# Kernel optimization log

Hardware: AMD Instinct MI355X
Metric: run time of the kernel (lower is better)

Reference implementation:

```python
import jax, jax.numpy as jnp
import numpy as np

N = 50000          # total points
C = 256            # channels
H = 8              # heads
D = C // H         # head dim = 32
W = 256            # window size
STRIDE = 128
LENGTHS = [12500, 12500, 12500, 12500]
HID = 512          # ffn hidden = 2.0 * C
EPS = 1e-5


def _build_windows():
    """numpy port of build_windows_1d: returns (M, W) indices and bool mask."""
    idxs, masks = [], []
    start = 0
    for L in LENGTHS:
        n_windows = (L - 1) // STRIDE + 1
        for i in range(n_windows):
            s = i * STRIDE
            b = min(L, s + W)
            cur_len = b - s
            loc = np.arange(s, b, dtype=np.int32) + start
            if W - cur_len > 0:
                loc = np.concatenate([loc, np.full(W - cur_len, loc[-1], dtype=np.int32)])
            m = np.zeros(W, dtype=bool)
            m[:cur_len] = True
            idxs.append(loc)
            masks.append(m)
        start += L
    return np.stack(idxs, 0), np.stack(masks, 0)


def setup_inputs() -> dict:
    key = jax.random.key(0)
    ks = jax.random.split(key, 8)
    def p(k, shape):
        return jax.random.normal(k, shape, dtype=jnp.float32) * 0.02
    win_idx_np, win_mask_np = _build_windows()
    return {
        "x": jax.random.normal(ks[0], (N, C), dtype=jnp.float32),
        "win_idx": jnp.asarray(win_idx_np, dtype=jnp.int32),
        "win_mask": jnp.asarray(win_mask_np),
        "norm1_g": jnp.ones((C,), jnp.float32), "norm1_b": jnp.zeros((C,), jnp.float32),
        "qkv_w": p(ks[1], (C, 3 * C)),
        "proj_w": p(ks[2], (C, C)), "proj_b": jnp.zeros((C,), jnp.float32),
        "ca_norm_g": jnp.ones((C,), jnp.float32), "ca_norm_b": jnp.zeros((C,), jnp.float32),
        "ca_qkv_w": p(ks[3], (C, 3 * C)), "ca_qkv_b": jnp.zeros((3 * C,), jnp.float32),
        "ca_proj_w": p(ks[4], (C, C)), "ca_proj_b": jnp.zeros((C,), jnp.float32),
        "norm2_g": jnp.ones((C,), jnp.float32), "norm2_b": jnp.zeros((C,), jnp.float32),
        "ffn_w1": p(ks[5], (C, HID)), "ffn_b1": jnp.zeros((HID,), jnp.float32),
        "ffn_ln_g": jnp.ones((HID,), jnp.float32), "ffn_ln_b": jnp.zeros((HID,), jnp.float32),
        "ffn_w2": p(ks[6], (HID, C)), "ffn_b2": jnp.zeros((C,), jnp.float32),
    }


def _ln(x, g, b):
    m = jnp.mean(x, axis=-1, keepdims=True)
    v = jnp.mean((x - m) ** 2, axis=-1, keepdims=True)
    return (x - m) * jax.lax.rsqrt(v + EPS) * g + b


def reference(x, win_idx, win_mask,
              norm1_g, norm1_b, qkv_w, proj_w, proj_b,
              ca_norm_g, ca_norm_b, ca_qkv_w, ca_qkv_b, ca_proj_w, ca_proj_b,
              norm2_g, norm2_b, ffn_w1, ffn_b1, ffn_ln_g, ffn_ln_b, ffn_w2, ffn_b2):
    M, Wn = win_idx.shape
    scale = D ** -0.5
    maskf = win_mask[..., None].astype(x.dtype)          # [M, W, 1]

    x_in = _ln(x, norm1_g, norm1_b)                      # [N, C]
    xw = x_in[win_idx]                                   # gather windows [M, W, C]

    # --- Stream A: per-window SDPA ---
    qkv = xw @ qkv_w                                     # [M, W, 3C]
    q, k, v = [t.reshape(M, Wn, H, D).transpose(0, 2, 1, 3)
               for t in jnp.split(qkv, 3, axis=-1)]      # each [M, H, W, D]
    scores = jnp.einsum('mhqd,mhkd->mhqk', q, k) * scale
    scores = jnp.where(win_mask[:, None, None, :], scores, -jnp.inf)
    attn = jax.nn.softmax(scores, axis=-1)
    out = jnp.einsum('mhqk,mhkd->mhqd', attn, v).transpose(0, 2, 1, 3).reshape(M, Wn, C)
    out = (out @ proj_w + proj_b) * maskf                # masked per-window output

    # --- Stream B: centroid attention over M window centroids ---
    wc = jnp.maximum(win_mask.sum(-1, keepdims=True).astype(x.dtype), 1.0)  # [M, 1]
    cent = (xw * maskf).sum(1) / wc                      # [M, C]
    cx = _ln(cent, ca_norm_g, ca_norm_b)
    cqkv = cx @ ca_qkv_w + ca_qkv_b
    cq, ck, cv = [t.reshape(M, H, D).transpose(1, 0, 2)
                  for t in jnp.split(cqkv, 3, axis=-1)]  # each [H, M, D]
    cs = jnp.einsum('hqd,hkd->hqk', cq, ck) * scale
    co = jnp.einsum('hqk,hkd->hqd', jax.nn.softmax(cs, -1), cv)
    co = co.transpose(1, 0, 2).reshape(M, C)
    cent_out = cent + co @ ca_proj_w + ca_proj_b         # residual + proj

    gctx = cent_out[:, None, :] * maskf                  # broadcast global ctx [M, W, C]

    # --- scatter-add back with overlap averaging ---
    total = (out + gctx).reshape(-1, C)
    flat_idx = win_idx.reshape(-1)
    y = jnp.zeros_like(x).at[flat_idx].add(total)
    counts = jnp.zeros((x.shape[0], 1), x.dtype).at[flat_idx].add(
        win_mask.reshape(-1, 1).astype(x.dtype))
    x_out = x + y / jnp.maximum(counts, 1.0)

    # --- FFN (LayerNorm variant) ---
    h1 = _ln(x_out, norm2_g, norm2_b) @ ffn_w1 + ffn_b1
    h1 = jax.nn.relu(_ln(h1, ffn_ln_g, ffn_ln_b))
    return x_out + h1 @ ffn_w2 + ffn_b2
```

## Files before the change

### kernel.cpp

```cpp
#include <hip/hip_runtime.h>

typedef unsigned short ushort;
typedef unsigned int uint;
typedef __attribute__((ext_vector_type(4))) float f32x4;
typedef __attribute__((ext_vector_type(16))) float f32x16;
typedef __attribute__((ext_vector_type(8))) short bf16x8;
typedef __attribute__((ext_vector_type(4))) uint uint32x4;
typedef __attribute__((ext_vector_type(2))) uint uint2v;

#define NPTS 50000
#define C 256
#define CH3 768
#define H 8
#define D 32
#define WW 256
#define HID 512
#define EPSV 1e-5f
#define QK_SCALE 0.17677669529663687f
#define LOG2E 1.4426950408889634f
#define SC_LOG2 (QK_SCALE * LOG2E)

#define BM 128
#define BN 128
#define BK 64
#define NGEMM_QKV 2346
#define NCENT 392
#define NATT 3136
#define NPROJ 1568

#if __has_builtin(__builtin_amdgcn_exp2f)
#define EXP2R(x) __builtin_amdgcn_exp2f(x)
#else
#define EXP2R(x) exp2f(x)
#endif

__device__ inline float bf2f(ushort u) { uint i = ((uint)u) << 16; float f; __builtin_memcpy(&f, &i, 4); return f; }
__device__ inline float bflo(uint u) { uint i = u << 16; float f; __builtin_memcpy(&f, &i, 4); return f; }
__device__ inline float bfhi(uint u) { uint i = u & 0xffff0000u; float f; __builtin_memcpy(&f, &i, 4); return f; }
__device__ inline ushort f2bf(float f) {
  uint i; __builtin_memcpy(&i, &f, 4);
  uint r = i + 0x7fffu + ((i >> 16) & 1u);
  return (ushort)(r >> 16);
}
__device__ inline uint pk2bf(float a, float b) { return (uint)f2bf(a) | ((uint)f2bf(b) << 16); }

__device__ __forceinline__ void gload16(const ushort* g, const ushort* l) {
  __builtin_amdgcn_global_load_lds(
      (const __attribute__((address_space(1))) unsigned int*)(unsigned long long)g,
      (__attribute__((address_space(3))) unsigned int*)(unsigned int)(unsigned long long)l,
      16, 0, 0);
}

__device__ __forceinline__ int xcd_swz(int orig, int nwg) {
  int q8 = nwg >> 3, r8 = nwg & 7;
  int xcd = orig & 7, sub = orig >> 3;
  return (xcd < r8 ? xcd * (q8 + 1) : r8 * (q8 + 1) + (xcd - r8) * q8) + sub;
}

#define BLOCK_REDUCE_2(sv, s2v)                                            \
  {                                                                        \
    _Pragma("unroll")                                                      \
    for (int o_ = 1; o_ < 64; o_ <<= 1) {                                  \
      sv  += __shfl_xor(sv, o_);                                           \
      s2v += __shfl_xor(s2v, o_);                                          \
    }                                                                      \
    __shared__ float ls_[4], ls2_[4];                                      \
    int wid_ = threadIdx.x >> 6;                                           \
    if ((threadIdx.x & 63) == 0) { ls_[wid_] = sv; ls2_[wid_] = s2v; }     \
    __syncthreads();                                                       \
    sv  = ls_[0] + ls_[1] + ls_[2] + ls_[3];                               \
    s2v = ls2_[0] + ls2_[1] + ls2_[2] + ls2_[3];                           \
  }

template <int EPI>
__device__ __forceinline__ void gemm_body(ushort* SMEM, int bid,
                                          const ushort* __restrict__ A,
                                          const ushort* __restrict__ Bt,
                                          void* __restrict__ outp,
                                          const float* __restrict__ bias,
                                          int Mrows, int Ncols, int K) {
  ushort* As = SMEM;
  ushort* Bs = SMEM + BM * BK;
  int t = threadIdx.x;
  int nbn = Ncols >> 7;
  int bm = bid / nbn, bn = bid - bm * nbn;
  int l = t & 63, wv = t >> 6;
  int wr = wv >> 1, wcid = wv & 1;
  int l15 = l & 15, l4 = l >> 4;
  int lr = l >> 3;
  int csrc = ((l & 7) ^ lr) << 3;
  f32x4 acc[4][4];
#pragma unroll
  for (int i = 0; i < 4; ++i)
#pragma unroll
    for (int j = 0; j < 4; ++j) acc[i][j] = (f32x4){0.f, 0.f, 0.f, 0.f};

  int nks = K >> 6;
  for (int ks = 0; ks < nks; ++ks) {
    if (ks) __syncthreads();
#pragma unroll
    for (int i = 0; i < 4; ++i) {
      int rloc = wv * 8 + lr + i * 32;
      int growA = min(bm * BM + rloc, Mrows - 1);
      gload16(&A[(size_t)growA * K + (ks << 6) + csrc], &As[(wv * 8 + i * 32) * BK]);
      gload16(&Bt[(size_t)(bn * BN + rloc) * K + (ks << 6) + csrc], &Bs[(wv * 8 + i * 32) * BK]);
    }
    __syncthreads();
#pragma unroll
    for (int kk = 0; kk < 2; ++kk) {
      bf16x8 af[4], bfr[4];
#pragma unroll
      for (int i = 0; i < 4; ++i) {
        int ra = wr * 64 + i * 16 + l15;
        int ca = (l4 + kk * 4) ^ (ra & 7);
        af[i] = *(const bf16x8*)&As[ra * BK + (ca << 3)];
        int rb = wcid * 64 + i * 16 + l15;
        int cb = (l4 + kk * 4) ^ (rb & 7);
        bfr[i] = *(const bf16x8*)&Bs[rb * BK + (cb << 3)];
      }
      __builtin_amdgcn_s_setprio(1);
#pragma unroll
      for (int i = 0; i < 4; ++i)
#pragma unroll
        for (int j = 0; j < 4; ++j)
          acc[i][j] = __builtin_amdgcn_mfma_f32_16x16x32_bf16(af[i], bfr[j], acc[i][j], 0, 0, 0);
      __builtin_amdgcn_s_setprio(0);
    }
  }

  const int CS = 136;
  ushort* Cs = SMEM;
#pragma unroll
  for (int pass = 0; pass < 2; ++pass) {
    __syncthreads();
    if (wr == pass) {
#pragma unroll
      for (int i = 0; i < 4; ++i)
#pragma unroll
        for (int j = 0; j < 4; ++j)
#pragma unroll
          for (int r = 0; r < 4; ++r) {
            int rl = i * 16 + l4 * 4 + r;
            int cl = wcid * 64 + j * 16 + l15;
            float v = acc[i][j][r];
            if (EPI >= 1) v += bias[bn * BN + cl];
            Cs[rl * CS + cl] = f2bf(v);
          }
    }
    __syncthreads();
    int rl = t >> 2;
    int cq = (t & 3) * 32;
    int grow = bm * BM + pass * 64 + rl;
    if (grow < Mrows) {
      if (EPI <= 1) {
        ushort* orow = (ushort*)outp + (size_t)grow * Ncols + bn * BN + cq;
#pragma unroll
        for (int s = 0; s < 4; ++s)
          *(uint4*)(orow + s * 8) = *(const uint4*)&Cs[rl * CS + cq + s * 8];
      } else {
        float* orow = (float*)outp + (size_t)grow * Ncols + bn * BN + cq;
#pragma unroll
        for (int s = 0; s < 8; ++s) {
          float4 ov = *(float4*)(orow + s * 4);
          const ushort* cp = &Cs[rl * CS + cq + s * 4];
          ov.x += bf2f(cp[0]); ov.y += bf2f(cp[1]);
          ov.z += bf2f(cp[2]); ov.w += bf2f(cp[3]);
          *(float4*)(orow + s * 4) = ov;
        }
      }
    }
  }
}

template <int EPI>
__global__ __launch_bounds__(256, 4) void gemm_bf16(
    const ushort* __restrict__ A, const ushort* __restrict__ Bt, void* __restrict__ outp,
    const float* __restrict__ bias, int Mrows, int Ncols, int K) {
  __shared__ ushort SMEM[(BM + BN) * BK];
  int bid = xcd_swz(blockIdx.x, gridDim.x);
  gemm_body<EPI>(SMEM, bid, A, Bt, outp, bias, Mrows, Ncols, K);
}

__global__ __launch_bounds__(256) void pre_kernel(
    const float* __restrict__ qkv_w, const float* __restrict__ proj_w,
    const float* __restrict__ w1, const float* __restrict__ w2,
    ushort* __restrict__ qkv_wt, ushort* __restrict__ proj_wt,
    ushort* __restrict__ w1t, ushort* __restrict__ w2t,
    const float* __restrict__ x, const float* __restrict__ g, const float* __restrict__ b,
    ushort* __restrict__ xout) {
  int bid = blockIdx.x;
  if (bid < 128) {
    __shared__ float tile[64][65];
    const float* w; ushort* wt; int K, N, boff; float scale; int n_hi;
    if (bid < 48)      { w = qkv_w;  wt = qkv_wt;  K = C;   N = CH3; boff = 0;  scale = SC_LOG2; n_hi = C; }
    else if (bid < 64) { w = proj_w; wt = proj_wt; K = C;   N = C;   boff = 48; scale = 1.f; n_hi = 0; }
    else if (bid < 96) { w = w1;     wt = w1t;     K = C;   N = HID; boff = 64; scale = 1.f; n_hi = 0; }
    else               { w = w2;     wt = w2t;     K = HID; N = C;   boff = 96; scale = 1.f; n_hi = 0; }
    int lb = bid - boff;
    int nbn = N >> 6;
    int bk = lb / nbn, bn = lb - bk * nbn;
    int c = threadIdx.x & 63, r4 = threadIdx.x >> 6;
#pragma unroll
    for (int rr = 0; rr < 16; ++rr) {
      int r = rr * 4 + r4;
      tile[r][c] = w[(size_t)(bk * 64 + r) * N + bn * 64 + c];
    }
    __syncthreads();
#pragma unroll
    for (int rr = 0; rr < 16; ++rr) {
      int r = rr * 4 + r4;
      int n = bn * 64 + r;
      float s = (n < n_hi) ? scale : 1.f;
      wt[(size_t)n * K + bk * 64 + c] = f2bf(tile[c][r] * s);
    }
  } else {
    int wv = threadIdx.x >> 6, lane = threadIdx.x & 63;
    int row = (bid - 128) * 4 + wv;
    float4 v = ((const float4*)(x + (size_t)row * C))[lane];
    float s = v.x + v.y + v.z + v.w;
    float s2 = v.x * v.x + v.y * v.y + v.z * v.z + v.w * v.w;
#pragma unroll
    for (int o = 1; o < 64; o <<= 1) { s += __shfl_xor(s, o); s2 += __shfl_xor(s2, o); }
    float mean = s * (1.0f / C);
    float var = s2 * (1.0f / C) - mean * mean;
    float rs = rsqrtf(var + EPSV);
    float4 gv = ((const float4*)g)[lane];
    float4 bv = ((const float4*)b)[lane];
    uint2 pk;
    pk.x = pk2bf((v.x - mean) * rs * gv.x + bv.x, (v.y - mean) * rs * gv.y + bv.y);
    pk.y = pk2bf((v.z - mean) * rs * gv.z + bv.z, (v.w - mean) * rs * gv.w + bv.w);
    ((uint2*)(xout + (size_t)row * C))[lane] = pk;
  }
}

__global__ __launch_bounds__(256, 4) void qkv_cent_kernel(
    const ushort* __restrict__ xb, const int* __restrict__ win_idx,
    const float* __restrict__ lng, const float* __restrict__ lnb,
    const float* __restrict__ caw, const float* __restrict__ cab,
    float* __restrict__ cent, float* __restrict__ cqkv, float* __restrict__ kT,
    int* __restrict__ wc_i, const ushort* __restrict__ qkv_wt, ushort* __restrict__ qkvb, int M) {
  __shared__ ushort SMEM[(BM + BN) * BK];
  int bid = blockIdx.x;
  if (bid < NCENT) {
    float* fbase = (float*)SMEM;
    float (*red)[257] = (float(*)[257])fbase;
    float* cxl = fbase + 8 * 257;
    int m = bid, t = threadIdx.x;
    int i0 = win_idx[m * WW];
    int iL = win_idx[m * WW + WW - 1];
    int wc = iL - i0 + 1;
    if (t == 0) wc_i[m] = wc;
    int rg = t >> 5, cg = t & 31;
    float acc[8] = {0.f, 0.f, 0.f, 0.f, 0.f, 0.f, 0.f, 0.f};
    for (int r = rg; r < wc; r += 8) {
      uint4 u = *(const uint4*)(xb + (size_t)(i0 + r) * C + cg * 8);
      acc[0] += bflo(u.x); acc[1] += bfhi(u.x);
      acc[2] += bflo(u.y); acc[3] += bfhi(u.y);
      acc[4] += bflo(u.z); acc[5] += bfhi(u.z);
      acc[6] += bflo(u.w); acc[7] += bfhi(u.w);
    }
#pragma unroll
    for (int j = 0; j < 8; ++j) red[rg][cg * 8 + j] = acc[j];
    __syncthreads();
    float sum = red[0][t];
#pragma unroll
    for (int k = 1; k < 8; ++k) sum += red[k][t];
    float cv = sum / (float)wc;
    cent[m * C + t] = cv;
    float s = cv, s2 = cv * cv;
    BLOCK_REDUCE_2(s, s2);
    float mean = s * (1.0f / C);
    float var = s2 * (1.0f / C) - mean * mean;
    float rs = rsqrtf(var + EPSV);
    cxl[t] = (cv - mean) * rs * lng[t] + lnb[t];
    __syncthreads();
    for (int j = t; j < CH3; j += 256) {
      float a = cab[j];
      for (int c2 = 0; c2 < C; ++c2) a += cxl[c2] * caw[(size_t)c2 * CH3 + j];
      cqkv[(size_t)m * CH3 + j] = a;
      if (j >= C && j < 2 * C) kT[(size_t)(j - C) * M + m] = a;
    }
  } else {
    int g = xcd_swz(bid - NCENT, NGEMM_QKV);
    gemm_body<0>(SMEM, g, xb, qkv_wt, qkvb, nullptr, NPTS, CH3, C);
  }
}

__global__ __launch_bounds__(256) void attn_cent_kernel(
    const ushort* __restrict__ qkv, const int* __restrict__ win_idx,
    const int* __restrict__ wc_i, ushort* __restrict__ ao,
    const float* __restrict__ cqkv, const float* __restrict__ kT,
    float* __restrict__ co, int* __restrict__ slots, int M) {
  __shared__ char SM[37376];
  int bid = blockIdx.x;
  int t = threadIdx.x;

  if (bid < NCENT) {
    float (*p_lds)[400] = (float(*)[400])(float*)SM;
    int wv = t >> 6, lane = t & 63;
    int mq = bid;
#pragma unroll
    for (int pp = 0; pp < 2; ++pp) {
      int h = wv * 2 + pp;
      const float* qp = cqkv + (size_t)mq * CH3 + h * D;
      float q[D];
#pragma unroll
      for (int d = 0; d < D; ++d) q[d] = qp[d] * SC_LOG2;
      float s[7];
      float mi = -3.0e38f;
#pragma unroll
      for (int j = 0; j < 7; ++j) {
        int mk = lane + 64 * j;
        s[j] = -3.0e38f;
        if (mk < M) {
          float a = 0.f;
#pragma unroll
          for (int d = 0; d < D; ++d) a += q[d] * kT[(size_t)(h * D + d) * M + mk];
          s[j] = a;
          mi = fmaxf(mi, a);
        }
      }
#pragma unroll
      for (int off = 1; off < 64; off <<= 1) mi = fmaxf(mi, __shfl_xor(mi, off));
      float li = 0.f;
#pragma unroll
      for (int j = 0; j < 7; ++j) {
        int mk = lane + 64 * j;
        if (mk < M) { float pv = EXP2R(s[j] - mi); li += pv; p_lds[h][mk] = pv; }
      }
#pragma unroll
      for (int off = 1; off < 64; off <<= 1) li += __shfl_xor(li, off);
      int d = lane & 31, hpp = lane >> 5;
      int half = (M + 1) / 2;
      int k0 = hpp * half, k1 = min(M, k0 + half);
      float o = 0.f;
      for (int k = k0; k < k1; ++k)
        o += p_lds[h][k] * cqkv[(size_t)k * CH3 + 2 * C + h * D + d];
      o += __shfl_xor(o, 32);
      if (lane < 32) co[(size_t)mq * C + h * D + d] = o / li;
    }
    return;
  }
  if (bid < 2 * NCENT) {
    int m = bid - NCENT;
    int wc = wc_i[m];
    int i0 = win_idx[m * WW];
    if (t < wc) slots[2 * (i0 + t) + (t >= 128 ? 0 : 1)] = m * WW + t;
    return;
  }

  ushort* K_lds = (ushort*)SM;
  uint* Vt = (uint*)(SM + 20480);
  int abid = xcd_swz(bid - 2 * NCENT, NATT);
  int m = abid >> 3, h = abid & 7;
  int wcv = wc_i[m];
  int i0 = win_idx[m * WW];
  int lane = t & 63, wq = t >> 6;
  int l31 = lane & 31, hp = lane >> 5;

  bf16x8 qf[2][2];
#pragma unroll
  for (int qb = 0; qb < 2; ++qb) {
    int qrow = i0 + min(wq * 64 + qb * 32 + l31, wcv - 1);
#pragma unroll
    for (int c = 0; c < 2; ++c)
      qf[qb][c] = *(const bf16x8*)(qkv + (size_t)qrow * CH3 + h * D + c * 16 + hp * 8);
  }

  if (t >= 128) {
    int base = (t - 128) * 2;
#pragma unroll
    for (int rr = 0; rr < 2; ++rr) {
      int row = base + rr;
      const uint4* src = (const uint4*)(qkv + (size_t)(i0 + min(row, wcv - 1)) * CH3 + C + h * D);
      *(uint4*)&K_lds[row * 40 + 0]  = src[0];
      *(uint4*)&K_lds[row * 40 + 8]  = src[1];
      *(uint4*)&K_lds[row * 40 + 16] = src[2];
      *(uint4*)&K_lds[row * 40 + 24] = src[3];
    }
  } else {
    int k0 = t * 2;
    const uint* s0 = (const uint*)(qkv + (size_t)(i0 + min(k0, wcv - 1)) * CH3 + 2 * C + h * D);
    const uint* s1 = (const uint*)(qkv + (size_t)(i0 + min(k0 + 1, wcv - 1)) * CH3 + 2 * C + h * D);
#pragma unroll
    for (int w2 = 0; w2 < 16; ++w2) {
      uint a = s0[w2], b = s1[w2];
      Vt[(2 * w2) * 132 + t] = (a & 0xffffu) | (b << 16);
      Vt[(2 * w2 + 1) * 132 + t] = (a >> 16) | (b & 0xffff0000u);
    }
  }
  __syncthreads();

  const f32x16 zv = {0.f, 0.f, 0.f, 0.f, 0.f, 0.f, 0.f, 0.f,
                     0.f, 0.f, 0.f, 0.f, 0.f, 0.f, 0.f, 0.f};
  f32x16 O0 = zv, O1 = zv;
  float l0 = 0.f, l1 = 0.f;
  int ntile = (wcv + 31) >> 5;

  for (int kt = 0; kt < ntile; ++kt) {
    int kbase = kt * 32;
    bf16x8 ka0 = *(const bf16x8*)&K_lds[(kbase + l31) * 40 + hp * 8];
    bf16x8 ka1 = *(const bf16x8*)&K_lds[(kbase + l31) * 40 + 16 + hp * 8];
    uint4 v0raw = *(const uint4*)&Vt[l31 * 132 + kt * 16 + hp * 4];
    uint4 v1raw = *(const uint4*)&Vt[l31 * 132 + kt * 16 + 8 + hp * 4];
    bf16x8 vb0 = __builtin_bit_cast(bf16x8, v0raw);
    bf16x8 vb1 = __builtin_bit_cast(bf16x8, v1raw);
    bool partial = (kbase + 32 > wcv);

    auto qbody = [&](const bf16x8& q0, const bf16x8& q1, f32x16& O, float& lq) {
      __builtin_amdgcn_s_setprio(1);
      f32x16 st = __builtin_amdgcn_mfma_f32_32x32x16_bf16(ka0, q0, zv, 0, 0, 0);
      st = __builtin_amdgcn_mfma_f32_32x32x16_bf16(ka1, q1, st, 0, 0, 0);
      __builtin_amdgcn_s_setprio(0);
      if (partial) {
        int kb_h = kbase + 4 * hp;
#pragma unroll
        for (int r = 0; r < 16; ++r) {
          int crow = (r & 3) + 8 * (r >> 2);
          st[r] = (kb_h + crow >= wcv) ? -3.0e38f : st[r];
        }
      }
      float p[16];
      float ls = 0.f;
#pragma unroll
      for (int r = 0; r < 16; ++r) { p[r] = EXP2R(st[r]); ls += p[r]; }
      lq += ls;
      uint w[8];
#pragma unroll
      for (int i = 0; i < 8; ++i) {
        uint o;
        asm("v_cvt_pk_bf16_f32 %0, %1, %2" : "=v"(o) : "v"(p[2 * i]), "v"(p[2 * i + 1]));
        w[i] = o;
      }
#if __has_builtin(__builtin_amdgcn_permlane32_swap)
      uint2v s02 = __builtin_amdgcn_permlane32_swap(w[0], w[2], false, false);
      uint2v s13 = __builtin_amdgcn_permlane32_swap(w[1], w[3], false, false);
      uint2v s46 = __builtin_amdgcn_permlane32_swap(w[4], w[6], false, false);
      uint2v s57 = __builtin_amdgcn_permlane32_swap(w[5], w[7], false, false);
      uint32x4 pa0u = {s02.x, s13.x, s02.y, s13.y};
      uint32x4 pa1u = {s46.x, s57.x, s46.y, s57.y};
#else
      uint sw0 = __shfl_xor((int)w[0], 32), sw1 = __shfl_xor((int)w[1], 32);
      uint sw2 = __shfl_xor((int)w[2], 32), sw3 = __shfl_xor((int)w[3], 32);
      uint sw4 = __shfl_xor((int)w[4], 32), sw5 = __shfl_xor((int)w[5], 32);
      uint sw6 = __shfl_xor((int)w[6], 32), sw7 = __shfl_xor((int)w[7], 32);
      uint32x4 pa0u = {hp ? sw2 : w[0], hp ? sw3 : w[1], hp ? w[2] : sw0, hp ? w[3] : sw1};
      uint32x4 pa1u = {hp ? sw6 : w[4], hp ? sw7 : w[5], hp ? w[6] : sw4, hp ? w[7] : sw5};
#endif
      bf16x8 pa0 = __builtin_bit_cast(bf16x8, pa0u);
      bf16x8 pa1 = __builtin_bit_cast(bf16x8, pa1u);
      __builtin_amdgcn_s_setprio(1);
      O = __builtin_amdgcn_mfma_f32_32x32x16_bf16(pa0, vb0, O, 0, 0, 0);
      O = __builtin_amdgcn_mfma_f32_32x32x16_bf16(pa1, vb1, O, 0, 0, 0);
      __builtin_amdgcn_s_setprio(0);
    };
    qbody(qf[0][0], qf[0][1], O0, l0);
    qbody(qf[1][0], qf[1][1], O1, l1);
  }

  auto epi = [&](f32x16& O, float lq, int qb) {
    float lt = lq + __shfl_xor(lq, 32);
    float inv = 1.f / lt;
#pragma unroll
    for (int r = 0; r < 16; ++r) {
      int qi = (r & 3) + 8 * (r >> 2) + 4 * hp;
      float iv = __shfl(inv, qi);
      int row = m * WW + wq * 64 + qb * 32 + qi;
      ao[(size_t)row * C + h * D + l31] = f2bf(O[r] * iv);
    }
  };
  epi(O0, l0, 0);
  epi(O1, l1, 1);
}

__global__ __launch_bounds__(256, 4) void proj_cent_kernel(
    const ushort* __restrict__ aob, const ushort* __restrict__ proj_wt,
    ushort* __restrict__ pout, const float* __restrict__ proj_b,
    const float* __restrict__ co, const float* __restrict__ cent,
    const float* __restrict__ pw, const float* __restrict__ pb,
    float* __restrict__ cent_o, int M) {
  __shared__ ushort SMEM[(BM + BN) * BK];
  int bid = blockIdx.x;
  if (bid < NCENT) {
    float* co_lds = (float*)SMEM;
    int mq = bid, t = threadIdx.x;
    co_lds[t] = co[(size_t)mq * C + t];
    __syncthreads();
    float a = pb[t] + cent[(size_t)mq * C + t];
    for (int k = 0; k < C; ++k) a += co_lds[k] * pw[(size_t)k * C + t];
    cent_o[(size_t)mq * C + t] = a;
    return;
  }
  int g = xcd_swz(bid - NCENT, NPROJ);
  gemm_body<1>(SMEM, g, aob, proj_wt, pout, proj_b, M * WW, C, C);
}

__global__ __launch_bounds__(256) void combine_ln_kernel(
    const float* __restrict__ x, const int* __restrict__ slots,
    const ushort* __restrict__ pout, const float* __restrict__ cent_o,
    const float* __restrict__ g, const float* __restrict__ b,
    float* __restrict__ xout, ushort* __restrict__ lnx) {
  int wv = threadIdx.x >> 6, lane = threadIdx.x & 63;
  int i = blockIdx.x * 4 + wv;
  int e0 = slots[2 * i], e1 = slots[2 * i + 1];
  float4 xv = ((const float4*)(x + (size_t)i * C))[lane];
  float a0 = 0.f, a1 = 0.f, a2 = 0.f, a3 = 0.f, cnt = 0.f;
  if (e0 >= 0) {
    uint2 pv = ((const uint2*)(pout + (size_t)e0 * C))[lane];
    float4 cv = ((const float4*)(cent_o + (size_t)(e0 >> 8) * C))[lane];
    a0 += bflo(pv.x) + cv.x; a1 += bfhi(pv.x) + cv.y;
    a2 += bflo(pv.y) + cv.z; a3 += bfhi(pv.y) + cv.w;
    cnt += 1.f;
  }
  if (e1 >= 0) {
    uint2 pv = ((const uint2*)(pout + (size_t)e1 * C))[lane];
    float4 cv = ((const float4*)(cent_o + (size_t)(e1 >> 8) * C))[lane];
    a0 += bflo(pv.x) + cv.x; a1 += bfhi(pv.x) + cv.y;
    a2 += bflo(pv.y) + cv.z; a3 += bfhi(pv.y) + cv.w;
    cnt += 1.f;
  }
  float inv = cnt > 0.f ? 1.f / cnt : 0.f;
  float o0 = xv.x + a0 * inv, o1 = xv.y + a1 * inv;
  float o2 = xv.z + a2 * inv, o3 = xv.w + a3 * inv;
  float s = o0 + o1 + o2 + o3;
  float s2 = o0 * o0 + o1 * o1 + o2 * o2 + o3 * o3;
#pragma unroll
  for (int o = 1; o < 64; o <<= 1) { s += __shfl_xor(s, o); s2 += __shfl_xor(s2, o); }
  float mean = s * (1.0f / C);
  float var = s2 * (1.0f / C) - mean * mean;
  float rs = rsqrtf(var + EPSV);
  ((float4*)(xout + (size_t)i * C))[lane] = make_float4(o0, o1, o2, o3);
  float4 gv = ((const float4*)g)[lane];
  float4 bv = ((const float4*)b)[lane];
  uint2 pk;
  pk.x = pk2bf((o0 - mean) * rs * gv.x + bv.x, (o1 - mean) * rs * gv.y + bv.y);
  pk.y = pk2bf((o2 - mean) * rs * gv.z + bv.z, (o3 - mean) * rs * gv.w + bv.w);
  ((uint2*)(lnx + (size_t)i * C))[lane] = pk;
}

__global__ __launch_bounds__(256) void hln_relu_kernel(ushort* __restrict__ h,
                                                       const float* __restrict__ g,
                                                       const float* __restrict__ b) {
  int wv = threadIdx.x >> 6, lane = threadIdx.x & 63;
  int i = blockIdx.x * 4 + wv;
  uint4 u = ((const uint4*)(h + (size_t)i * HID))[lane];
  float v[8] = {bflo(u.x), bfhi(u.x), bflo(u.y), bfhi(u.y),
                bflo(u.z), bfhi(u.z), bflo(u.w), bfhi(u.w)};
  float s = 0.f, s2 = 0.f;
#pragma unroll
  for (int j = 0; j < 8; ++j) { s += v[j]; s2 += v[j] * v[j]; }
#pragma unroll
  for (int o = 1; o < 64; o <<= 1) { s += __shfl_xor(s, o); s2 += __shfl_xor(s2, o); }
  float mean = s * (1.0f / HID);
  float var = s2 * (1.0f / HID) - mean * mean;
  float rs = rsqrtf(var + EPSV);
  float4 g0 = ((const float4*)g)[lane * 2], g1 = ((const float4*)g)[lane * 2 + 1];
  float4 b0 = ((const float4*)b)[lane * 2], b1 = ((const float4*)b)[lane * 2 + 1];
  float ga[8] = {g0.x, g0.y, g0.z, g0.w, g1.x, g1.y, g1.z, g1.w};
  float ba[8] = {b0.x, b0.y, b0.z, b0.w, b1.x, b1.y, b1.z, b1.w};
  float r[8];
#pragma unroll
  for (int j = 0; j < 8; ++j) r[j] = fmaxf((v[j] - mean) * rs * ga[j] + ba[j], 0.f);
  uint4 outu = make_uint4(pk2bf(r[0], r[1]), pk2bf(r[2], r[3]),
                          pk2bf(r[4], r[5]), pk2bf(r[6], r[7]));
  ((uint4*)(h + (size_t)i * HID))[lane] = outu;
}

extern "C" void kernel_launch(void* const* d_in, const int* in_sizes, int n_in,
                              void* d_out, int out_size, void* d_ws, size_t ws_size,
                              hipStream_t stream) {
  (void)n_in; (void)ws_size; (void)out_size;
  const float* x         = (const float*)d_in[0];
  const int*   win_idx   = (const int*)d_in[1];
  const float* norm1_g   = (const float*)d_in[3];
  const float* norm1_b   = (const float*)d_in[4];
  const float* qkv_w     = (const float*)d_in[5];
  const float* proj_w    = (const float*)d_in[6];
  const float* proj_b    = (const float*)d_in[7];
  const float* ca_norm_g = (const float*)d_in[8];
  const float* ca_norm_b = (const float*)d_in[9];
  const float* ca_qkv_w  = (const float*)d_in[10];
  const float* ca_qkv_b  = (const float*)d_in[11];
  const float* ca_proj_w = (const float*)d_in[12];
  const float* ca_proj_b = (const float*)d_in[13];
  const float* norm2_g   = (const float*)d_in[14];
  const float* norm2_b   = (const float*)d_in[15];
  const float* ffn_w1    = (const float*)d_in[16];
  const float* ffn_b1    = (const float*)d_in[17];
  const float* ffn_ln_g  = (const float*)d_in[18];
  const float* ffn_ln_b  = (const float*)d_in[19];
  const float* ffn_w2    = (const float*)d_in[20];
  const float* ffn_b2    = (const float*)d_in[21];

  const int M = in_sizes[1] / WW;

  char* p = (char*)d_ws;
  auto alloc = [&](size_t bytes) { char* r = p; p += (bytes + 255) & ~(size_t)255; return r; };
  ushort* x_in_b = (ushort*)alloc((size_t)NPTS * C * 2);
  ushort* qkvb   = (ushort*)alloc((size_t)NPTS * CH3 * 2);
  ushort* aob    = (ushort*)alloc((size_t)M * WW * C * 2);
  ushort* pout   = (ushort*)alloc((size_t)M * WW * C * 2);
  int*   slots   = (int*)  alloc((size_t)NPTS * 2 * 4);
  int*   wc_i    = (int*)  alloc((size_t)M * 4);
  float* cent    = (float*)alloc((size_t)M * C * 4);
  float* cqkv    = (float*)alloc((size_t)M * CH3 * 4);
  float* kT      = (float*)alloc((size_t)C * M * 4);
  float* co      = (float*)alloc((size_t)M * C * 4);
  float* cent_o  = (float*)alloc((size_t)M * C * 4);
  ushort* qkv_wt = (ushort*)alloc((size_t)CH3 * C * 2);
  ushort* proj_wt= (ushort*)alloc((size_t)C * C * 2);
  ushort* w1t    = (ushort*)alloc((size_t)HID * C * 2);
  ushort* w2t    = (ushort*)alloc((size_t)C * HID * 2);
  float* yout    = (float*)d_out;

  hipMemsetAsync(slots, 0xFF, (size_t)NPTS * 2 * 4, stream);

  pre_kernel<<<128 + NPTS / 4, 256, 0, stream>>>(
      qkv_w, proj_w, ffn_w1, ffn_w2, qkv_wt, proj_wt, w1t, w2t,
      x, norm1_g, norm1_b, x_in_b);

  qkv_cent_kernel<<<NCENT + NGEMM_QKV, 256, 0, stream>>>(
      x_in_b, win_idx, ca_norm_g, ca_norm_b, ca_qkv_w, ca_qkv_b,
      cent, cqkv, kT, wc_i, qkv_wt, qkvb, M);

  attn_cent_kernel<<<2 * NCENT + NATT, 256, 0, stream>>>(
      qkvb, win_idx, wc_i, aob, cqkv, kT, co, slots, M);

  proj_cent_kernel<<<NCENT + NPROJ, 256, 0, stream>>>(
      aob, proj_wt, pout, proj_b, co, cent, ca_proj_w, ca_proj_b, cent_o, M);

  ushort* lnx = x_in_b;
  combine_ln_kernel<<<NPTS / 4, 256, 0, stream>>>(x, slots, pout, cent_o, norm2_g, norm2_b,
                                                  yout, lnx);
  ushort* h1 = qkvb;
  const int gm = (NPTS + BM - 1) / BM;
  gemm_bf16<1><<<gm * (HID / BN), 256, 0, stream>>>(lnx, w1t, h1, ffn_b1,
                                                    NPTS, HID, C);
  hln_relu_kernel<<<NPTS / 4, 256, 0, stream>>>(h1, ffn_ln_g, ffn_ln_b);
  gemm_bf16<2><<<gm * (C / BN), 256, 0, stream>>>(h1, w2t, yout, ffn_b2,
                                                  NPTS, C, HID);
}
```

Before: 387.8 us.

## Use 512-thread blocks in window attention, one 32-query tile per wave

Doubles the attention kernel's block size to 512 threads so each of 8 waves handles one 32-row query tile (instead of 4 waves with two tiles each). The centroid branch now gives each wave a single head rather than looping over two. K and V staging is split across more threads. This raises parallelism and cuts per-wave serial work and register pressure, at the cost of more threads per block and fewer independent MFMA chains per wave for latency hiding. The slot-writing branch now has idle threads.

```diff
diff --git a/kernel.cpp b/kernel.cpp
--- a/kernel.cpp
+++ b/kernel.cpp
@@ -286,7 +286,7 @@
   }
 }
 
-__global__ __launch_bounds__(256) void attn_cent_kernel(
+__global__ __launch_bounds__(512) void attn_cent_kernel(
     const ushort* __restrict__ qkv, const int* __restrict__ win_idx,
     const int* __restrict__ wc_i, ushort* __restrict__ ao,
     const float* __restrict__ cqkv, const float* __restrict__ kT,
@@ -294,51 +294,49 @@
   __shared__ char SM[37376];
   int bid = blockIdx.x;
   int t = threadIdx.x;
+  int wavei = t >> 6, lane = t & 63;
+  int l31 = lane & 31, hp = lane >> 5;
 
   if (bid < NCENT) {
     float (*p_lds)[400] = (float(*)[400])(float*)SM;
-    int wv = t >> 6, lane = t & 63;
     int mq = bid;
-#pragma unroll
-    for (int pp = 0; pp < 2; ++pp) {
-      int h = wv * 2 + pp;
-      const float* qp = cqkv + (size_t)mq * CH3 + h * D;
-      float q[D];
-#pragma unroll
-      for (int d = 0; d < D; ++d) q[d] = qp[d] * SC_LOG2;
-      float s[7];
-      float mi = -3.0e38f;
-#pragma unroll
-      for (int j = 0; j < 7; ++j) {
-        int mk = lane + 64 * j;
-        s[j] = -3.0e38f;
-        if (mk < M) {
-          float a = 0.f;
-#pragma unroll
-          for (int d = 0; d < D; ++d) a += q[d] * kT[(size_t)(h * D + d) * M + mk];
-          s[j] = a;
-          mi = fmaxf(mi, a);
-        }
+    int h = wavei;
+    const float* qp = cqkv + (size_t)mq * CH3 + h * D;
+    float q[D];
+#pragma unroll
+    for (int d = 0; d < D; ++d) q[d] = qp[d] * SC_LOG2;
+    float s[7];
+    float mi = -3.0e38f;
+#pragma unroll
+    for (int j = 0; j < 7; ++j) {
+      int mk = lane + 64 * j;
+      s[j] = -3.0e38f;
+      if (mk < M) {
+        float a = 0.f;
+#pragma unroll
+        for (int d = 0; d < D; ++d) a += q[d] * kT[(size_t)(h * D + d) * M + mk];
+        s[j] = a;
+        mi = fmaxf(mi, a);
       }
-#pragma unroll
-      for (int off = 1; off < 64; off <<= 1) mi = fmaxf(mi, __shfl_xor(mi, off));
-      float li = 0.f;
-#pragma unroll
-      for (int j = 0; j < 7; ++j) {
-        int mk = lane + 64 * j;
-        if (mk < M) { float pv = EXP2R(s[j] - mi); li += pv; p_lds[h][mk] = pv; }
-      }
-#pragma unroll
-      for (int off = 1; off < 64; off <<= 1) li += __shfl_xor(li, off);
-      int d = lane & 31, hpp = lane >> 5;
-      int half = (M + 1) / 2;
-      int k0 = hpp * half, k1 = min(M, k0 + half);
-      float o = 0.f;
-      for (int k = k0; k < k1; ++k)
-        o += p_lds[h][k] * cqkv[(size_t)k * CH3 + 2 * C + h * D + d];
-      o += __shfl_xor(o, 32);
-      if (lane < 32) co[(size_t)mq * C + h * D + d] = o / li;
-    }
+    }
+#pragma unroll
+    for (int off = 1; off < 64; off <<= 1) mi = fmaxf(mi, __shfl_xor(mi, off));
+    float li = 0.f;
+#pragma unroll
+    for (int j = 0; j < 7; ++j) {
+      int mk = lane + 64 * j;
+      if (mk < M) { float pv = EXP2R(s[j] - mi); li += pv; p_lds[h][mk] = pv; }
+    }
+#pragma unroll
+    for (int off = 1; off < 64; off <<= 1) li += __shfl_xor(li, off);
+    int d = lane & 31, hpp = lane >> 5;
+    int half = (M + 1) / 2;
+    int k0 = hpp * half, k1 = min(M, k0 + half);
+    float o = 0.f;
+    for (int k = k0; k < k1; ++k)
+      o += p_lds[h][k] * cqkv[(size_t)k * CH3 + 2 * C + h * D + d];
+    o += __shfl_xor(o, 32);
+    if (lane < 32) co[(size_t)mq * C + h * D + d] = o / li;
     return;
   }
   if (bid < 2 * NCENT) {
@@ -355,30 +353,22 @@
   int m = abid >> 3, h = abid & 7;
   int wcv = wc_i[m];
   int i0 = win_idx[m * WW];
-  int lane = t & 63, wq = t >> 6;
-  int l31 = lane & 31, hp = lane >> 5;
-
-  bf16x8 qf[2][2];
-#pragma unroll
-  for (int qb = 0; qb < 2; ++qb) {
-    int qrow = i0 + min(wq * 64 + qb * 32 + l31, wcv - 1);
-#pragma unroll
-    for (int c = 0; c < 2; ++c)
-      qf[qb][c] = *(const bf16x8*)(qkv + (size_t)qrow * CH3 + h * D + c * 16 + hp * 8);
-  }
-
-  if (t >= 128) {
-    int base = (t - 128) * 2;
-#pragma unroll
-    for (int rr = 0; rr < 2; ++rr) {
-      int row = base + rr;
-      const uint4* src = (const uint4*)(qkv + (size_t)(i0 + min(row, wcv - 1)) * CH3 + C + h * D);
-      *(uint4*)&K_lds[row * 40 + 0]  = src[0];
-      *(uint4*)&K_lds[row * 40 + 8]  = src[1];
-      *(uint4*)&K_lds[row * 40 + 16] = src[2];
-      *(uint4*)&K_lds[row * 40 + 24] = src[3];
-    }
-  } else {
+
+  bf16x8 qf0, qf1;
+  {
+    int qrow = i0 + min(wavei * 32 + l31, wcv - 1);
+    qf0 = *(const bf16x8*)(qkv + (size_t)qrow * CH3 + h * D + hp * 8);
+    qf1 = *(const bf16x8*)(qkv + (size_t)qrow * CH3 + h * D + 16 + hp * 8);
+  }
+
+  if (t >= 256) {
+    int row = t - 256;
+    const uint4* src = (const uint4*)(qkv + (size_t)(i0 + min(row, wcv - 1)) * CH3 + C + h * D);
+    *(uint4*)&K_lds[row * 40 + 0]  = src[0];
+    *(uint4*)&K_lds[row * 40 + 8]  = src[1];
+    *(uint4*)&K_lds[row * 40 + 16] = src[2];
+    *(uint4*)&K_lds[row * 40 + 24] = src[3];
+  } else if (t < 128) {
     int k0 = t * 2;
     const uint* s0 = (const uint*)(qkv + (size_t)(i0 + min(k0, wcv - 1)) * CH3 + 2 * C + h * D);
     const uint* s1 = (const uint*)(qkv + (size_t)(i0 + min(k0 + 1, wcv - 1)) * CH3 + 2 * C + h * D);
@@ -393,84 +383,76 @@
 
   const f32x16 zv = {0.f, 0.f, 0.f, 0.f, 0.f, 0.f, 0.f, 0.f,
                      0.f, 0.f, 0.f, 0.f, 0.f, 0.f, 0.f, 0.f};
-  f32x16 O0 = zv, O1 = zv;
-  float l0 = 0.f, l1 = 0.f;
+  f32x16 O = zv;
+  float lq = 0.f;
   int ntile = (wcv + 31) >> 5;
 
   for (int kt = 0; kt < ntile; ++kt) {
     int kbase = kt * 32;
-    bf16x8 ka0 = *(const bf16x8*)&K_lds[(kbase + l31) * 40 + hp * 8];
-    bf16x8 ka1 = *(const bf16x8*)&K_lds[(kbase + l31) * 40 + 16 + hp * 8];
+    int rowk = kbase + l31;
+    bf16x8 ka0 = *(const bf16x8*)&K_lds[rowk * 40 + hp * 8];
+    bf16x8 ka1 = *(const bf16x8*)&K_lds[rowk * 40 + 16 + hp * 8];
     uint4 v0raw = *(const uint4*)&Vt[l31 * 132 + kt * 16 + hp * 4];
     uint4 v1raw = *(const uint4*)&Vt[l31 * 132 + kt * 16 + 8 + hp * 4];
     bf16x8 vb0 = __builtin_bit_cast(bf16x8, v0raw);
     bf16x8 vb1 = __builtin_bit_cast(bf16x8, v1raw);
     bool partial = (kbase + 32 > wcv);
 
-    auto qbody = [&](const bf16x8& q0, const bf16x8& q1, f32x16& O, float& lq) {
-      __builtin_amdgcn_s_setprio(1);
-      f32x16 st = __builtin_amdgcn_mfma_f32_32x32x16_bf16(ka0, q0, zv, 0, 0, 0);
-      st = __builtin_amdgcn_mfma_f32_32x32x16_bf16(ka1, q1, st, 0, 0, 0);
-      __builtin_amdgcn_s_setprio(0);
-      if (partial) {
-        int kb_h = kbase + 4 * hp;
-#pragma unroll
-        for (int r = 0; r < 16; ++r) {
-          int crow = (r & 3) + 8 * (r >> 2);
-          st[r] = (kb_h + crow >= wcv) ? -3.0e38f : st[r];
-        }
+    __builtin_amdgcn_s_setprio(1);
+    f32x16 st = __builtin_amdgcn_mfma_f32_32x32x16_bf16(ka0, qf0, zv, 0, 0, 0);
+    st = __builtin_amdgcn_mfma_f32_32x32x16_bf16(ka1, qf1, st, 0, 0, 0);
+    __builtin_amdgcn_s_setprio(0);
+    if (partial) {
+      int kb_h = kbase + 4 * hp;
+#pragma unroll
+      for (int r = 0; r < 16; ++r) {
+        int crow = (r & 3) + 8 * (r >> 2);
+        st[r] = (kb_h + crow >= wcv) ? -3.0e38f : st[r];
       }
-      float p[16];
-      float ls = 0.f;
-#pragma unroll
-      for (int r = 0; r < 16; ++r) { p[r] = EXP2R(st[r]); ls += p[r]; }
-      lq += ls;
-      uint w[8];
-#pragma unroll
-      for (int i = 0; i < 8; ++i) {
-        uint o;
-        asm("v_cvt_pk_bf16_f32 %0, %1, %2" : "=v"(o) : "v"(p[2 * i]), "v"(p[2 * i + 1]));
-        w[i] = o;
-      }
+    }
+    float ls = 0.f;
+#pragma unroll
+    for (int r = 0; r < 16; ++r) { st[r] = EXP2R(st[r]); ls += st[r]; }
+    lq += ls;
+    uint w[8];
+#pragma unroll
+    for (int i = 0; i < 8; ++i) {
+      uint o;
+      asm("v_cvt_pk_bf16_f32 %0, %1, %2" : "=v"(o) : "v"(st[2 * i]), "v"(st[2 * i + 1]));
+      w[i] = o;
+    }
 #if __has_builtin(__builtin_amdgcn_permlane32_swap)
-      uint2v s02 = __builtin_amdgcn_permlane32_swap(w[0], w[2], false, false);
-      uint2v s13 = __builtin_amdgcn_permlane32_swap(w[1], w[3], false, false);
-      uint2v s46 = __builtin_amdgcn_permlane32_swap(w[4], w[6], false, false);
-      uint2v s57 = __builtin_amdgcn_permlane32_swap(w[5], w[7], false, false);
-      uint32x4 pa0u = {s02.x, s13.x, s02.y, s13.y};
-      uint32x4 pa1u = {s46.x, s57.x, s46.y, s57.y};
+    uint2v s02 = __builtin_amdgcn_permlane32_swap(w[0], w[2], false, false);
+    uint2v s13 = __builtin_amdgcn_permlane32_swap(w[1], w[3], false, false);
+    uint2v s46 = __builtin_amdgcn_permlane32_swap(w[4], w[6], false, false);
+    uint2v s57 = __builtin_amdgcn_permlane32_swap(w[5], w[7], false, false);
+    uint32x4 pa0u = {s02.x, s13.x, s02.y, s13.y};
+    uint32x4 pa1u = {s46.x, s57.x, s46.y, s57.y};
 #else
-      uint sw0 = __shfl_xor((int)w[0], 32), sw1 = __shfl_xor((int)w[1], 32);
-      uint sw2 = __shfl_xor((int)w[2], 32), sw3 = __shfl_xor((int)w[3], 32);
-      uint sw4 = __shfl_xor((int)w[4], 32), sw5 = __shfl_xor((int)w[5], 32);
-      uint sw6 = __shfl_xor((int)w[6], 32), sw7 = __shfl_xor((int)w[7], 32);
-      uint32x4 pa0u = {hp ? sw2 : w[0], hp ? sw3 : w[1], hp ? w[2] : sw0, hp ? w[3] : sw1};
-      uint32x4 pa1u = {hp ? sw6 : w[4], hp ? sw7 : w[5], hp ? w[6] : sw4, hp ? w[7] : sw5};
+    uint sw0 = __shfl_xor((int)w[0], 32), sw1 = __shfl_xor((int)w[1], 32);
+    uint sw2 = __shfl_xor((int)w[2], 32), sw3 = __shfl_xor((int)w[3], 32);
+    uint sw4 = __shfl_xor((int)w[4], 32), sw5 = __shfl_xor((int)w[5], 32);
+    uint sw6 = __shfl_xor((int)w[6], 32), sw7 = __shfl_xor((int)w[7], 32);
+    uint32x4 pa0u = {hp ? sw2 : w[0], hp ? sw3 : w[1], hp ? w[2] : sw0, hp ? w[3] : sw1};
+    uint32x4 pa1u = {hp ? sw6 : w[4], hp ? sw7 : w[5], hp ? w[6] : sw4, hp ? w[7] : sw5};
 #endif
-      bf16x8 pa0 = __builtin_bit_cast(bf16x8, pa0u);
-      bf16x8 pa1 = __builtin_bit_cast(bf16x8, pa1u);
-      __builtin_amdgcn_s_setprio(1);
-      O = __builtin_amdgcn_mfma_f32_32x32x16_bf16(pa0, vb0, O, 0, 0, 0);
-      O = __builtin_amdgcn_mfma_f32_32x32x16_bf16(pa1, vb1, O, 0, 0, 0);
-      __builtin_amdgcn_s_setprio(0);
-    };
-    qbody(qf[0][0], qf[0][1], O0, l0);
-    qbody(qf[1][0], qf[1][1], O1, l1);
-  }
-
-  auto epi = [&](f32x16& O, float lq, int qb) {
-    float lt = lq + __shfl_xor(lq, 32);
-    float inv = 1.f / lt;
-#pragma unroll
-    for (int r = 0; r < 16; ++r) {
-      int qi = (r & 3) + 8 * (r >> 2) + 4 * hp;
-      float iv = __shfl(inv, qi);
-      int row = m * WW + wq * 64 + qb * 32 + qi;
-      ao[(size_t)row * C + h * D + l31] = f2bf(O[r] * iv);
-    }
-  };
-  epi(O0, l0, 0);
-  epi(O1, l1, 1);
+    bf16x8 pa0 = __builtin_bit_cast(bf16x8, pa0u);
+    bf16x8 pa1 = __builtin_bit_cast(bf16x8, pa1u);
+    __builtin_amdgcn_s_setprio(1);
+    O = __builtin_amdgcn_mfma_f32_32x32x16_bf16(pa0, vb0, O, 0, 0, 0);
+    O = __builtin_amdgcn_mfma_f32_32x32x16_bf16(pa1, vb1, O, 0, 0, 0);
+    __builtin_amdgcn_s_setprio(0);
+  }
+
+  float lt = lq + __shfl_xor(lq, 32);
+  float inv = 1.f / lt;
+#pragma unroll
+  for (int r = 0; r < 16; ++r) {
+    int qi = (r & 3) + 8 * (r >> 2) + 4 * hp;
+    float iv = __shfl(inv, qi);
+    int row = m * WW + wavei * 32 + qi;
+    ao[(size_t)row * C + h * D + l31] = f2bf(O[r] * iv);
+  }
 }
 
 __global__ __launch_bounds__(256, 4) void proj_cent_kernel(
@@ -623,7 +605,7 @@
       x_in_b, win_idx, ca_norm_g, ca_norm_b, ca_qkv_w, ca_qkv_b,
       cent, cqkv, kT, wc_i, qkv_wt, qkvb, M);
 
-  attn_cent_kernel<<<2 * NCENT + NATT, 256, 0, stream>>>(
+  attn_cent_kernel<<<2 * NCENT + NATT, 512, 0, stream>>>(
       qkvb, win_idx, wc_i, aob, cqkv, kT, co, slots, M);
 
   proj_cent_kernel<<<NCENT + NPROJ, 256, 0, stream>>>(
```

Measured after the change: 386.3 us. No clear change (-0.4%).
